# Kernel tuning notes

Hardware: AMD Instinct MI355X
Metric: run time of the kernel (lower is better)

Reference implementation:

```python
import jax, jax.numpy as jnp
import numpy as np

NUM_NODES = 500000
DIM = 128
BATCH = 131072
MOMENTUM = 0.9


def setup_inputs() -> dict:
    key = jax.random.key(0)
    ks = jax.random.split(key, 6)
    s = 1.0 / np.sqrt(DIM)
    return {
        "hidden": jax.random.normal(ks[0], (NUM_NODES, DIM), jnp.float32),
        "variance": jnp.ones((NUM_NODES, DIM), jnp.float32),
        "idx": jnp.arange(BATCH, dtype=jnp.int64 if jax.config.jax_enable_x64 else jnp.int32),
        "new_repr": jax.random.normal(ks[1], (BATCH, DIM), jnp.float32),
        "W_ih": jax.random.normal(ks[2], (3 * DIM, DIM), jnp.float32) * s,
        "W_hh": jax.random.normal(ks[3], (3 * DIM, DIM), jnp.float32) * s,
        "b_ih": jax.random.normal(ks[4], (3 * DIM,), jnp.float32) * s,
        "b_hh": jax.random.normal(ks[5], (3 * DIM,), jnp.float32) * s,
    }


def _gru_cell(x, h, W_ih, W_hh, b_ih, b_hh):
    # torch GRUCell gate layout: [reset | update | new], each of size DIM
    gi = x @ W_ih.T + b_ih          # [B, 3*DIM]
    gh = h @ W_hh.T + b_hh          # [B, 3*DIM]
    gi_r, gi_z, gi_n = jnp.split(gi, 3, axis=-1)
    gh_r, gh_z, gh_n = jnp.split(gh, 3, axis=-1)
    r = jax.nn.sigmoid(gi_r + gh_r)
    z = jax.nn.sigmoid(gi_z + gh_z)
    n = jnp.tanh(gi_n + r * gh_n)
    return (1.0 - z) * n + z * h


def reference(hidden, variance, idx, new_repr, W_ih, W_hh, b_ih, b_hh):
    h_prev = hidden[idx]                                   # gather [B, DIM]
    h_new = _gru_cell(new_repr, h_prev, W_ih, W_hh, b_ih, b_hh)
    delta = h_new - h_prev
    var_new = MOMENTUM * variance[idx] + (1.0 - MOMENTUM) * delta * delta
    hidden_out = hidden.at[idx].set(h_new)                 # scatter write
    variance_out = variance.at[idx].set(var_new)
    return jnp.stack([hidden_out, variance_out])           # [2, N, DIM]
```

## Files before the change

### kernel.cpp

```cpp
#include <hip/hip_runtime.h>
#include <hip/hip_bf16.h>
#include <cstdint>
#include <cstddef>

#define NUM_NODES 500000
#define DIM 128
#define BATCH 131072
#define NBLK (NUM_NODES / 32)

typedef __attribute__((ext_vector_type(8))) short short8;
typedef __attribute__((ext_vector_type(4))) short short4_t;
typedef __attribute__((ext_vector_type(4))) float f32x4;

static __device__ __forceinline__ short f2bf(float f) {
    unsigned u = __builtin_bit_cast(unsigned, f);
    u += 0x7fffu + ((u >> 16) & 1u);
    return (short)(u >> 16);
}
static __device__ __forceinline__ float bf2f(short s) {
    unsigned u = ((unsigned)(unsigned short)s) << 16;
    return __builtin_bit_cast(float, u);
}
static __device__ __forceinline__ f32x4 ntl(const float* p) {
    return __builtin_nontemporal_load((const f32x4*)p);
}
static __device__ __forceinline__ void nts(float* p, f32x4 v) {
    __builtin_nontemporal_store(v, (f32x4*)p);
}

__global__ void k_init(int* __restrict__ inv,
                       unsigned char* __restrict__ mask,
                       const float* __restrict__ Wih,
                       const float* __restrict__ Whh,
                       short* __restrict__ WbIH,
                       short* __restrict__ WbHH) {
    int i = blockIdx.x * blockDim.x + threadIdx.x;
    if (i < NUM_NODES) {
        if (inv)  inv[i] = -1;
        if (mask) mask[i] = 0;
    }
    if (i < 3 * DIM * DIM) {
        WbIH[i] = f2bf(Wih[i]);
        WbHH[i] = f2bf(Whh[i]);
    }
}

__global__ void k_scatter(int* __restrict__ inv, unsigned char* __restrict__ mask,
                          const int* __restrict__ idx) {
    int i = blockIdx.x * blockDim.x + threadIdx.x;
    if (i < BATCH) {
        int n = idx[i];
        if (inv)  inv[n] = i;
        if (mask) mask[n] = 1;
    }
}

__global__ void __launch_bounds__(512)
k_stream(const float* __restrict__ hidden,
         const float* __restrict__ variance,
         const int*   __restrict__ inv,
         const float* __restrict__ xg,
         const short* __restrict__ WbIH,
         const short* __restrict__ WbHH,
         const float* __restrict__ b_ih,
         const float* __restrict__ b_hh,
         float* __restrict__ out0,
         float* __restrict__ out1) {
    __shared__ __align__(16) char smem[26112];
    short (*Xb)[136] = (short(*)[136])smem;
    short (*Hb)[136] = (short(*)[136])(smem + 8704);
    short (*Vb)[136] = (short(*)[136])(smem + 17408);
    short (*Hn)[136] = (short(*)[136])smem;
    __shared__ int rinfo[32];
    __shared__ int hasUpd;

    const int t  = threadIdx.x;
    const int pb = (int)(((unsigned)blockIdx.x * 4099u) % 15625u);
    const int rb = pb * 32;

    if (t == 0) hasUpd = 0;
    if (t < 32) rinfo[t] = inv[rb + t];
    __syncthreads();
    if (t < 32 && rinfo[t] >= 0) hasUpd = 1;
    __syncthreads();

    if (!hasUpd) {
        #pragma unroll
        for (int jj = 0; jj < 2; ++jj) {
            int j = t + jj * 512;
            size_t off = (size_t)rb * DIM + j * 4;
            f32x4 h = ntl(hidden + off);
            f32x4 v = ntl(variance + off);
            nts(out0 + off, h);
            nts(out1 + off, v);
        }
        return;
    }

    #pragma unroll
    for (int jj = 0; jj < 2; ++jj) {
        int j = t + jj * 512;
        int row = j >> 5, c4 = j & 31;
        size_t off = (size_t)(rb + row) * DIM + c4 * 4;
        f32x4 hv = ntl(hidden + off);
        f32x4 vv = ntl(variance + off);
        int iv = rinfo[row];
        f32x4 xv = {0.f, 0.f, 0.f, 0.f};
        if (iv >= 0) {
            xv = ntl(xg + (size_t)iv * DIM + c4 * 4);
        } else {
            nts(out0 + off, hv);
            nts(out1 + off, vv);
        }
        short4_t xs, hs, vs;
        xs.x = f2bf(xv.x); xs.y = f2bf(xv.y); xs.z = f2bf(xv.z); xs.w = f2bf(xv.w);
        hs.x = f2bf(hv.x); hs.y = f2bf(hv.y); hs.z = f2bf(hv.z); hs.w = f2bf(hv.w);
        vs.x = f2bf(vv.x); vs.y = f2bf(vv.y); vs.z = f2bf(vv.z); vs.w = f2bf(vv.w);
        *(short4_t*)&Xb[row][c4 * 4] = xs;
        *(short4_t*)&Hb[row][c4 * 4] = hs;
        *(short4_t*)&Vb[row][c4 * 4] = vs;
    }
    __syncthreads();

    const int w  = t >> 6;
    const int l  = t & 63;
    const int c  = l & 15;
    const int gq = l >> 4;

    f32x4 acc[2][3][2] = {};

    #pragma unroll
    for (int ks = 0; ks < 4; ++ks) {
        const int k0 = ks * 32 + gq * 8;
        short8 a[2][2];
        a[0][0] = *(const short8*)&Xb[c][k0];
        a[1][0] = *(const short8*)&Xb[16 + c][k0];
        a[0][1] = *(const short8*)&Hb[c][k0];
        a[1][1] = *(const short8*)&Hb[16 + c][k0];
        #pragma unroll
        for (int th = 0; th < 3; ++th) {
            const int o = w * 16 + th * 128 + c;
            const short8 bi = *(const short8*)(WbIH + (size_t)o * DIM + k0);
            const short8 bh = *(const short8*)(WbHH + (size_t)o * DIM + k0);
            #pragma unroll
            for (int mt = 0; mt < 2; ++mt) {
                acc[mt][th][0] = __builtin_amdgcn_mfma_f32_16x16x32_bf16(a[mt][0], bi, acc[mt][th][0], 0, 0, 0);
                acc[mt][th][1] = __builtin_amdgcn_mfma_f32_16x16x32_bf16(a[mt][1], bh, acc[mt][th][1], 0, 0, 0);
            }
        }
    }
    __syncthreads();

    const int d = w * 16 + c;
    const float bs_r = b_ih[d]       + b_hh[d];
    const float bs_z = b_ih[d + 128] + b_hh[d + 128];
    const float bi_n = b_ih[d + 256];
    const float bh_n = b_hh[d + 256];

    #pragma unroll
    for (int mt = 0; mt < 2; ++mt) {
        #pragma unroll
        for (int r = 0; r < 4; ++r) {
            const int m = mt * 16 + gq * 4 + r;
            float s_r  = acc[mt][0][0][r] + acc[mt][0][1][r] + bs_r;
            float s_z  = acc[mt][1][0][r] + acc[mt][1][1][r] + bs_z;
            float gi_n = acc[mt][2][0][r] + bi_n;
            float gh_n = acc[mt][2][1][r] + bh_n;
            float rg = 1.f / (1.f + __expf(-s_r));
            float zg = 1.f / (1.f + __expf(-s_z));
            float aa = gi_n + rg * gh_n;
            float n  = 1.f - 2.f / (__expf(2.f * aa) + 1.f);
            float h  = bf2f(Hb[m][d]);
            Hn[m][d] = f2bf((1.f - zg) * n + zg * h);
        }
    }
    __syncthreads();

    #pragma unroll
    for (int jj = 0; jj < 2; ++jj) {
        int j = t + jj * 512;
        int row = j >> 5, c4 = j & 31;
        if (rinfo[row] < 0) continue;
        size_t off = (size_t)(rb + row) * DIM + c4 * 4;
        short4_t hns = *(short4_t*)&Hn[row][c4 * 4];
        short4_t hs  = *(short4_t*)&Hb[row][c4 * 4];
        short4_t vs  = *(short4_t*)&Vb[row][c4 * 4];
        f32x4 hn, var;
        hn.x = bf2f(hns.x); hn.y = bf2f(hns.y); hn.z = bf2f(hns.z); hn.w = bf2f(hns.w);
        float dx = hn.x - bf2f(hs.x), dy = hn.y - bf2f(hs.y);
        float dz = hn.z - bf2f(hs.z), dw = hn.w - bf2f(hs.w);
        var.x = 0.9f * bf2f(vs.x) + 0.1f * dx * dx;
        var.y = 0.9f * bf2f(vs.y) + 0.1f * dy * dy;
        var.z = 0.9f * bf2f(vs.z) + 0.1f * dz * dz;
        var.w = 0.9f * bf2f(vs.w) + 0.1f * dw * dw;
        nts(out0 + off, hn);
        nts(out1 + off, var);
    }
}

__global__ void __launch_bounds__(256)
k_copy(const float* __restrict__ hidden,
       const float* __restrict__ variance,
       const unsigned char* __restrict__ mask,
       float* __restrict__ out0,
       float* __restrict__ out1) {
    int gid = blockIdx.x * 256 + threadIdx.x;
    int row = gid >> 4;
    int c8  = gid & 15;
    if (mask && mask[row]) return;
    size_t off = (size_t)row * DIM + c8 * 8;
    f32x4 a0 = *(const f32x4*)(hidden + off);
    f32x4 a1 = *(const f32x4*)(hidden + off + 4);
    f32x4 b0 = *(const f32x4*)(variance + off);
    f32x4 b1 = *(const f32x4*)(variance + off + 4);
    *(f32x4*)(out0 + off)     = a0;
    *(f32x4*)(out0 + off + 4) = a1;
    *(f32x4*)(out1 + off)     = b0;
    *(f32x4*)(out1 + off + 4) = b1;
}

__global__ void __launch_bounds__(512)
k_gru(const float* __restrict__ hidden,
      const float* __restrict__ variance,
      const int*   __restrict__ idx,
      const float* __restrict__ xg,
      const short* __restrict__ WbIH,
      const short* __restrict__ WbHH,
      const float* __restrict__ b_ih,
      const float* __restrict__ b_hh,
      float* __restrict__ out0,
      float* __restrict__ out1) {
    __shared__ __align__(16) char smem[26112];
    short (*Xb)[136] = (short(*)[136])smem;
    short (*Hb)[136] = (short(*)[136])(smem + 8704);
    short (*Vb)[136] = (short(*)[136])(smem + 17408);
    short (*Hn)[136] = (short(*)[136])smem;

    const int t  = threadIdx.x;
    const int rb = blockIdx.x * 32;

    #pragma unroll
    for (int jj = 0; jj < 2; ++jj) {
        int j = t + jj * 512;
        int row = j >> 5, c4 = j & 31;
        int node = idx[rb + row];
        f32x4 xv = *(const f32x4*)(xg + (size_t)(rb + row) * DIM + c4 * 4);
        f32x4 hv = *(const f32x4*)(hidden + (size_t)node * DIM + c4 * 4);
        f32x4 vv = *(const f32x4*)(variance + (size_t)node * DIM + c4 * 4);
        short4_t xs, hs, vs;
        xs.x = f2bf(xv.x); xs.y = f2bf(xv.y); xs.z = f2bf(xv.z); xs.w = f2bf(xv.w);
        hs.x = f2bf(hv.x); hs.y = f2bf(hv.y); hs.z = f2bf(hv.z); hs.w = f2bf(hv.w);
        vs.x = f2bf(vv.x); vs.y = f2bf(vv.y); vs.z = f2bf(vv.z); vs.w = f2bf(vv.w);
        *(short4_t*)&Xb[row][c4 * 4] = xs;
        *(short4_t*)&Hb[row][c4 * 4] = hs;
        *(short4_t*)&Vb[row][c4 * 4] = vs;
    }
    __syncthreads();

    const int w  = t >> 6;
    const int l  = t & 63;
    const int c  = l & 15;
    const int gq = l >> 4;

    f32x4 acc[2][3][2] = {};
    #pragma unroll
    for (int ks = 0; ks < 4; ++ks) {
        const int k0 = ks * 32 + gq * 8;
        short8 a[2][2];
        a[0][0] = *(const short8*)&Xb[c][k0];
        a[1][0] = *(const short8*)&Xb[16 + c][k0];
        a[0][1] = *(const short8*)&Hb[c][k0];
        a[1][1] = *(const short8*)&Hb[16 + c][k0];
        #pragma unroll
        for (int th = 0; th < 3; ++th) {
            const int o = w * 16 + th * 128 + c;
            const short8 bi = *(const short8*)(WbIH + (size_t)o * DIM + k0);
            const short8 bh = *(const short8*)(WbHH + (size_t)o * DIM + k0);
            #pragma unroll
            for (int mt = 0; mt < 2; ++mt) {
                acc[mt][th][0] = __builtin_amdgcn_mfma_f32_16x16x32_bf16(a[mt][0], bi, acc[mt][th][0], 0, 0, 0);
                acc[mt][th][1] = __builtin_amdgcn_mfma_f32_16x16x32_bf16(a[mt][1], bh, acc[mt][th][1], 0, 0, 0);
            }
        }
    }
    __syncthreads();

    const int d = w * 16 + c;
    const float bs_r = b_ih[d]       + b_hh[d];
    const float bs_z = b_ih[d + 128] + b_hh[d + 128];
    const float bi_n = b_ih[d + 256];
    const float bh_n = b_hh[d + 256];
    #pragma unroll
    for (int mt = 0; mt < 2; ++mt) {
        #pragma unroll
        for (int r = 0; r < 4; ++r) {
            const int m = mt * 16 + gq * 4 + r;
            float s_r  = acc[mt][0][0][r] + acc[mt][0][1][r] + bs_r;
            float s_z  = acc[mt][1][0][r] + acc[mt][1][1][r] + bs_z;
            float gi_n = acc[mt][2][0][r] + bi_n;
            float gh_n = acc[mt][2][1][r] + bh_n;
            float rg = 1.f / (1.f + __expf(-s_r));
            float zg = 1.f / (1.f + __expf(-s_z));
            float aa = gi_n + rg * gh_n;
            float n  = 1.f - 2.f / (__expf(2.f * aa) + 1.f);
            float h  = bf2f(Hb[m][d]);
            Hn[m][d] = f2bf((1.f - zg) * n + zg * h);
        }
    }
    __syncthreads();

    #pragma unroll
    for (int jj = 0; jj < 2; ++jj) {
        int j = t + jj * 512;
        int row = j >> 5, c4 = j & 31;
        int node = idx[rb + row];
        size_t off = (size_t)node * DIM + c4 * 4;
        short4_t hns = *(short4_t*)&Hn[row][c4 * 4];
        short4_t hs  = *(short4_t*)&Hb[row][c4 * 4];
        short4_t vs  = *(short4_t*)&Vb[row][c4 * 4];
        f32x4 hn, var;
        hn.x = bf2f(hns.x); hn.y = bf2f(hns.y); hn.z = bf2f(hns.z); hn.w = bf2f(hns.w);
        float dx = hn.x - bf2f(hs.x), dy = hn.y - bf2f(hs.y);
        float dz = hn.z - bf2f(hs.z), dw = hn.w - bf2f(hs.w);
        var.x = 0.9f * bf2f(vs.x) + 0.1f * dx * dx;
        var.y = 0.9f * bf2f(vs.y) + 0.1f * dy * dy;
        var.z = 0.9f * bf2f(vs.z) + 0.1f * dz * dz;
        var.w = 0.9f * bf2f(vs.w) + 0.1f * dw * dw;
        *(f32x4*)(out0 + off) = hn;
        *(f32x4*)(out1 + off) = var;
    }
}

extern "C" void kernel_launch(void* const* d_in, const int* in_sizes, int n_in,
                              void* d_out, int out_size, void* d_ws, size_t ws_size,
                              hipStream_t stream) {
    const float* hidden   = (const float*)d_in[0];
    const float* variance = (const float*)d_in[1];
    const int*   idx      = (const int*)d_in[2];
    const float* x        = (const float*)d_in[3];
    const float* Wih      = (const float*)d_in[4];
    const float* Whh      = (const float*)d_in[5];
    const float* bih      = (const float*)d_in[6];
    const float* bhh      = (const float*)d_in[7];
    float* out0 = (float*)d_out;
    float* out1 = out0 + (size_t)NUM_NODES * DIM;

    const size_t invB  = (size_t)NUM_NODES * 4;
    const size_t maskB = (size_t)NUM_NODES;
    const size_t wB    = (size_t)3 * DIM * DIM * 2;

    const bool full = ws_size >= invB + 2 * wB;
    const bool mid  = !full && ws_size >= maskB + 16 + 2 * wB;

    if (full) {
        int*   inv  = (int*)d_ws;
        short* WbIH = (short*)((char*)d_ws + invB);
        short* WbHH = WbIH + 3 * DIM * DIM;
        k_init<<<(NUM_NODES + 255) / 256, 256, 0, stream>>>(
            inv, nullptr, Wih, Whh, WbIH, WbHH);
        k_scatter<<<BATCH / 256, 256, 0, stream>>>(inv, nullptr, idx);
        k_stream<<<NBLK, 512, 0, stream>>>(hidden, variance, inv, x,
                                           WbIH, WbHH, bih, bhh, out0, out1);
    } else if (mid) {
        unsigned char* mask = (unsigned char*)d_ws;
        short* WbIH = (short*)((char*)d_ws + ((maskB + 15) & ~size_t(15)));
        short* WbHH = WbIH + 3 * DIM * DIM;
        k_init<<<(NUM_NODES + 255) / 256, 256, 0, stream>>>(
            nullptr, mask, Wih, Whh, WbIH, WbHH);
        k_scatter<<<BATCH / 256, 256, 0, stream>>>(nullptr, mask, idx);
        k_copy<<<(NUM_NODES * 16) / 256, 256, 0, stream>>>(
            hidden, variance, mask, out0, out1);
        k_gru<<<BATCH / 32, 512, 0, stream>>>(hidden, variance, idx, x,
                                              WbIH, WbHH, bih, bhh, out0, out1);
    } else {
        short* WbIH = (short*)d_ws;
        short* WbHH = WbIH + 3 * DIM * DIM;
        k_init<<<(NUM_NODES + 255) / 256, 256, 0, stream>>>(
            nullptr, nullptr, Wih, Whh, WbIH, WbHH);
        k_copy<<<(NUM_NODES * 16) / 256, 256, 0, stream>>>(
            hidden, variance, nullptr, out0, out1);
        k_gru<<<BATCH / 32, 512, 0, stream>>>(hidden, variance, idx, x,
                                              WbIH, WbHH, bih, bhh, out0, out1);
    }
}
```

Baseline: 253.2 us.

## Fuse GRU epilogue writes into MFMA output layout, drop variance staging

The GRU gate epilogue now writes h_new and the updated variance directly from the MFMA accumulator layout, reading fp32 hidden/variance from global memory per element. This removes the Vb shared buffer, the Hn staging pass and two block barriers. Variance is now loaded only for non-updated rows in the staging loop. The hidden load becomes a regular cached load so the epilogue re-read can hit cache. The trade-off is that stores become scalar and strided per lane (one float per row/column) instead of coalesced 16-byte stores, which may reduce write efficiency.

```diff
diff --git a/kernel.cpp b/kernel.cpp
--- a/kernel.cpp
+++ b/kernel.cpp
@@ -66,11 +66,8 @@
          const float* __restrict__ b_hh,
          float* __restrict__ out0,
          float* __restrict__ out1) {
-    __shared__ __align__(16) char smem[26112];
-    short (*Xb)[136] = (short(*)[136])smem;
-    short (*Hb)[136] = (short(*)[136])(smem + 8704);
-    short (*Vb)[136] = (short(*)[136])(smem + 17408);
-    short (*Hn)[136] = (short(*)[136])smem;
+    __shared__ __align__(16) short Xb[32][136];
+    __shared__ __align__(16) short Hb[32][136];
     __shared__ int rinfo[32];
     __shared__ int hasUpd;
 
@@ -102,23 +99,21 @@
         int j = t + jj * 512;
         int row = j >> 5, c4 = j & 31;
         size_t off = (size_t)(rb + row) * DIM + c4 * 4;
-        f32x4 hv = ntl(hidden + off);
-        f32x4 vv = ntl(variance + off);
+        f32x4 hv = *(const f32x4*)(hidden + off);
         int iv = rinfo[row];
         f32x4 xv = {0.f, 0.f, 0.f, 0.f};
         if (iv >= 0) {
             xv = ntl(xg + (size_t)iv * DIM + c4 * 4);
         } else {
+            f32x4 vv = ntl(variance + off);
             nts(out0 + off, hv);
             nts(out1 + off, vv);
         }
-        short4_t xs, hs, vs;
+        short4_t xs, hs;
         xs.x = f2bf(xv.x); xs.y = f2bf(xv.y); xs.z = f2bf(xv.z); xs.w = f2bf(xv.w);
         hs.x = f2bf(hv.x); hs.y = f2bf(hv.y); hs.z = f2bf(hv.z); hs.w = f2bf(hv.w);
-        vs.x = f2bf(vv.x); vs.y = f2bf(vv.y); vs.z = f2bf(vv.z); vs.w = f2bf(vv.w);
         *(short4_t*)&Xb[row][c4 * 4] = xs;
         *(short4_t*)&Hb[row][c4 * 4] = hs;
-        *(short4_t*)&Vb[row][c4 * 4] = vs;
     }
     __syncthreads();
 
@@ -149,7 +144,6 @@
             }
         }
     }
-    __syncthreads();
 
     const int d = w * 16 + c;
     const float bs_r = b_ih[d]       + b_hh[d];
@@ -162,6 +156,8 @@
         #pragma unroll
         for (int r = 0; r < 4; ++r) {
             const int m = mt * 16 + gq * 4 + r;
+            if (rinfo[m] < 0) continue;
+            size_t off = (size_t)(rb + m) * DIM + d;
             float s_r  = acc[mt][0][0][r] + acc[mt][0][1][r] + bs_r;
             float s_z  = acc[mt][1][0][r] + acc[mt][1][1][r] + bs_z;
             float gi_n = acc[mt][2][0][r] + bi_n;
@@ -170,31 +166,13 @@
             float zg = 1.f / (1.f + __expf(-s_z));
             float aa = gi_n + rg * gh_n;
             float n  = 1.f - 2.f / (__expf(2.f * aa) + 1.f);
-            float h  = bf2f(Hb[m][d]);
-            Hn[m][d] = f2bf((1.f - zg) * n + zg * h);
-        }
-    }
-    __syncthreads();
-
-    #pragma unroll
-    for (int jj = 0; jj < 2; ++jj) {
-        int j = t + jj * 512;
-        int row = j >> 5, c4 = j & 31;
-        if (rinfo[row] < 0) continue;
-        size_t off = (size_t)(rb + row) * DIM + c4 * 4;
-        short4_t hns = *(short4_t*)&Hn[row][c4 * 4];
-        short4_t hs  = *(short4_t*)&Hb[row][c4 * 4];
-        short4_t vs  = *(short4_t*)&Vb[row][c4 * 4];
-        f32x4 hn, var;
-        hn.x = bf2f(hns.x); hn.y = bf2f(hns.y); hn.z = bf2f(hns.z); hn.w = bf2f(hns.w);
-        float dx = hn.x - bf2f(hs.x), dy = hn.y - bf2f(hs.y);
-        float dz = hn.z - bf2f(hs.z), dw = hn.w - bf2f(hs.w);
-        var.x = 0.9f * bf2f(vs.x) + 0.1f * dx * dx;
-        var.y = 0.9f * bf2f(vs.y) + 0.1f * dy * dy;
-        var.z = 0.9f * bf2f(vs.z) + 0.1f * dz * dz;
-        var.w = 0.9f * bf2f(vs.w) + 0.1f * dw * dw;
-        nts(out0 + off, hn);
-        nts(out1 + off, var);
+            float h  = hidden[off];
+            float v  = __builtin_nontemporal_load(variance + off);
+            float hn = (1.f - zg) * n + zg * h;
+            float dl = hn - h;
+            __builtin_nontemporal_store(hn, out0 + off);
+            __builtin_nontemporal_store(0.9f * v + 0.1f * dl * dl, out1 + off);
+        }
     }
 }
 
```

Result: slower. 280.8 us (+10.9%).

## Process 64 rows per block, defer variance load, restructure gate-wise MFMA loop

Applied to the files above, without the earlier changes.

Doubles the tile to 64 node rows per block, so each weight fragment loaded from global memory feeds four M-tiles instead of two, and blocks become fewer and larger. Variance is no longer staged in LDS as bf16; updated rows read it directly from global memory in the epilogue, which also uses full-precision variance. The MFMA loop now runs one gate at a time, computing reset and update sigmoids as each finishes, which keeps the live accumulator set small despite the larger tile. In exchange, the mixed pass-through/update path covers more rows, a tail block with bounds checks is added, and the block permutation changes.

```diff
diff --git a/kernel.cpp b/kernel.cpp
--- a/kernel.cpp
+++ b/kernel.cpp
@@ -6,7 +6,8 @@
 #define NUM_NODES 500000
 #define DIM 128
 #define BATCH 131072
-#define NBLK (NUM_NODES / 32)
+#define ROWS 64
+#define NBLK ((NUM_NODES + ROWS - 1) / ROWS)
 
 typedef __attribute__((ext_vector_type(8))) short short8;
 typedef __attribute__((ext_vector_type(4))) short short4_t;
@@ -66,28 +67,26 @@
          const float* __restrict__ b_hh,
          float* __restrict__ out0,
          float* __restrict__ out1) {
-    __shared__ __align__(16) char smem[26112];
-    short (*Xb)[136] = (short(*)[136])smem;
-    short (*Hb)[136] = (short(*)[136])(smem + 8704);
-    short (*Vb)[136] = (short(*)[136])(smem + 17408);
-    short (*Hn)[136] = (short(*)[136])smem;
-    __shared__ int rinfo[32];
+    __shared__ __align__(16) short Xb[ROWS][136];
+    __shared__ __align__(16) short Hb[ROWS][136];
+    short (*Hn)[136] = Xb;
+    __shared__ int rinfo[ROWS];
     __shared__ int hasUpd;
 
     const int t  = threadIdx.x;
-    const int pb = (int)(((unsigned)blockIdx.x * 4099u) % 15625u);
-    const int rb = pb * 32;
+    const int pb = (int)(((unsigned)blockIdx.x * 2003u) % (unsigned)NBLK);
+    const int rb = pb * ROWS;
+    const int nrows = min(ROWS, NUM_NODES - rb);
 
     if (t == 0) hasUpd = 0;
-    if (t < 32) rinfo[t] = inv[rb + t];
-    __syncthreads();
-    if (t < 32 && rinfo[t] >= 0) hasUpd = 1;
+    if (t < ROWS) rinfo[t] = (t < nrows) ? inv[rb + t] : -1;
+    __syncthreads();
+    if (t < ROWS && rinfo[t] >= 0) hasUpd = 1;
     __syncthreads();
 
     if (!hasUpd) {
-        #pragma unroll
-        for (int jj = 0; jj < 2; ++jj) {
-            int j = t + jj * 512;
+        const int nchunks = nrows * 32;
+        for (int j = t; j < nchunks; j += 512) {
             size_t off = (size_t)rb * DIM + j * 4;
             f32x4 h = ntl(hidden + off);
             f32x4 v = ntl(variance + off);
@@ -98,27 +97,27 @@
     }
 
     #pragma unroll
-    for (int jj = 0; jj < 2; ++jj) {
+    for (int jj = 0; jj < 4; ++jj) {
         int j = t + jj * 512;
         int row = j >> 5, c4 = j & 31;
-        size_t off = (size_t)(rb + row) * DIM + c4 * 4;
-        f32x4 hv = ntl(hidden + off);
-        f32x4 vv = ntl(variance + off);
-        int iv = rinfo[row];
-        f32x4 xv = {0.f, 0.f, 0.f, 0.f};
-        if (iv >= 0) {
-            xv = ntl(xg + (size_t)iv * DIM + c4 * 4);
-        } else {
-            nts(out0 + off, hv);
-            nts(out1 + off, vv);
-        }
-        short4_t xs, hs, vs;
-        xs.x = f2bf(xv.x); xs.y = f2bf(xv.y); xs.z = f2bf(xv.z); xs.w = f2bf(xv.w);
-        hs.x = f2bf(hv.x); hs.y = f2bf(hv.y); hs.z = f2bf(hv.z); hs.w = f2bf(hv.w);
-        vs.x = f2bf(vv.x); vs.y = f2bf(vv.y); vs.z = f2bf(vv.z); vs.w = f2bf(vv.w);
+        short4_t xs = {0, 0, 0, 0}, hs = {0, 0, 0, 0};
+        if (row < nrows) {
+            size_t off = (size_t)(rb + row) * DIM + c4 * 4;
+            f32x4 hv = ntl(hidden + off);
+            int iv = rinfo[row];
+            f32x4 xv = {0.f, 0.f, 0.f, 0.f};
+            if (iv >= 0) {
+                xv = ntl(xg + (size_t)iv * DIM + c4 * 4);
+            } else {
+                f32x4 vv = ntl(variance + off);
+                nts(out0 + off, hv);
+                nts(out1 + off, vv);
+            }
+            xs.x = f2bf(xv.x); xs.y = f2bf(xv.y); xs.z = f2bf(xv.z); xs.w = f2bf(xv.w);
+            hs.x = f2bf(hv.x); hs.y = f2bf(hv.y); hs.z = f2bf(hv.z); hs.w = f2bf(hv.w);
+        }
         *(short4_t*)&Xb[row][c4 * 4] = xs;
         *(short4_t*)&Hb[row][c4 * 4] = hs;
-        *(short4_t*)&Vb[row][c4 * 4] = vs;
     }
     __syncthreads();
 
@@ -126,30 +125,6 @@
     const int l  = t & 63;
     const int c  = l & 15;
     const int gq = l >> 4;
-
-    f32x4 acc[2][3][2] = {};
-
-    #pragma unroll
-    for (int ks = 0; ks < 4; ++ks) {
-        const int k0 = ks * 32 + gq * 8;
-        short8 a[2][2];
-        a[0][0] = *(const short8*)&Xb[c][k0];
-        a[1][0] = *(const short8*)&Xb[16 + c][k0];
-        a[0][1] = *(const short8*)&Hb[c][k0];
-        a[1][1] = *(const short8*)&Hb[16 + c][k0];
-        #pragma unroll
-        for (int th = 0; th < 3; ++th) {
-            const int o = w * 16 + th * 128 + c;
-            const short8 bi = *(const short8*)(WbIH + (size_t)o * DIM + k0);
-            const short8 bh = *(const short8*)(WbHH + (size_t)o * DIM + k0);
-            #pragma unroll
-            for (int mt = 0; mt < 2; ++mt) {
-                acc[mt][th][0] = __builtin_amdgcn_mfma_f32_16x16x32_bf16(a[mt][0], bi, acc[mt][th][0], 0, 0, 0);
-                acc[mt][th][1] = __builtin_amdgcn_mfma_f32_16x16x32_bf16(a[mt][1], bh, acc[mt][th][1], 0, 0, 0);
-            }
-        }
-    }
-    __syncthreads();
 
     const int d = w * 16 + c;
     const float bs_r = b_ih[d]       + b_hh[d];
@@ -157,42 +132,71 @@
     const float bi_n = b_ih[d + 256];
     const float bh_n = b_hh[d + 256];
 
-    #pragma unroll
-    for (int mt = 0; mt < 2; ++mt) {
+    float rg[4][4], zg[4][4];
+
+    #pragma unroll
+    for (int th = 0; th < 3; ++th) {
+        f32x4 acc[4][2] = {};
+        const int o = w * 16 + th * 128 + c;
         #pragma unroll
-        for (int r = 0; r < 4; ++r) {
-            const int m = mt * 16 + gq * 4 + r;
-            float s_r  = acc[mt][0][0][r] + acc[mt][0][1][r] + bs_r;
-            float s_z  = acc[mt][1][0][r] + acc[mt][1][1][r] + bs_z;
-            float gi_n = acc[mt][2][0][r] + bi_n;
-            float gh_n = acc[mt][2][1][r] + bh_n;
-            float rg = 1.f / (1.f + __expf(-s_r));
-            float zg = 1.f / (1.f + __expf(-s_z));
-            float aa = gi_n + rg * gh_n;
-            float n  = 1.f - 2.f / (__expf(2.f * aa) + 1.f);
-            float h  = bf2f(Hb[m][d]);
-            Hn[m][d] = f2bf((1.f - zg) * n + zg * h);
-        }
-    }
-    __syncthreads();
-
-    #pragma unroll
-    for (int jj = 0; jj < 2; ++jj) {
+        for (int ks = 0; ks < 4; ++ks) {
+            const int k0 = ks * 32 + gq * 8;
+            const short8 bi = *(const short8*)(WbIH + (size_t)o * DIM + k0);
+            const short8 bh = *(const short8*)(WbHH + (size_t)o * DIM + k0);
+            #pragma unroll
+            for (int mt = 0; mt < 4; ++mt) {
+                const short8 aX = *(const short8*)&Xb[mt * 16 + c][k0];
+                const short8 aH = *(const short8*)&Hb[mt * 16 + c][k0];
+                acc[mt][0] = __builtin_amdgcn_mfma_f32_16x16x32_bf16(aX, bi, acc[mt][0], 0, 0, 0);
+                acc[mt][1] = __builtin_amdgcn_mfma_f32_16x16x32_bf16(aH, bh, acc[mt][1], 0, 0, 0);
+            }
+        }
+        if (th == 0) {
+            #pragma unroll
+            for (int mt = 0; mt < 4; ++mt)
+                #pragma unroll
+                for (int r = 0; r < 4; ++r)
+                    rg[mt][r] = 1.f / (1.f + __expf(-(acc[mt][0][r] + acc[mt][1][r] + bs_r)));
+        } else if (th == 1) {
+            #pragma unroll
+            for (int mt = 0; mt < 4; ++mt)
+                #pragma unroll
+                for (int r = 0; r < 4; ++r)
+                    zg[mt][r] = 1.f / (1.f + __expf(-(acc[mt][0][r] + acc[mt][1][r] + bs_z)));
+        } else {
+            __syncthreads();
+            #pragma unroll
+            for (int mt = 0; mt < 4; ++mt) {
+                #pragma unroll
+                for (int r = 0; r < 4; ++r) {
+                    const int m = mt * 16 + gq * 4 + r;
+                    float aa = (acc[mt][0][r] + bi_n) + rg[mt][r] * (acc[mt][1][r] + bh_n);
+                    float n  = 1.f - 2.f / (__expf(2.f * aa) + 1.f);
+                    float h  = bf2f(Hb[m][d]);
+                    Hn[m][d] = f2bf((1.f - zg[mt][r]) * n + zg[mt][r] * h);
+                }
+            }
+        }
+    }
+    __syncthreads();
+
+    #pragma unroll
+    for (int jj = 0; jj < 4; ++jj) {
         int j = t + jj * 512;
         int row = j >> 5, c4 = j & 31;
-        if (rinfo[row] < 0) continue;
+        if (row >= nrows || rinfo[row] < 0) continue;
         size_t off = (size_t)(rb + row) * DIM + c4 * 4;
         short4_t hns = *(short4_t*)&Hn[row][c4 * 4];
         short4_t hs  = *(short4_t*)&Hb[row][c4 * 4];
-        short4_t vs  = *(short4_t*)&Vb[row][c4 * 4];
+        f32x4 vv = ntl(variance + off);
         f32x4 hn, var;
         hn.x = bf2f(hns.x); hn.y = bf2f(hns.y); hn.z = bf2f(hns.z); hn.w = bf2f(hns.w);
         float dx = hn.x - bf2f(hs.x), dy = hn.y - bf2f(hs.y);
         float dz = hn.z - bf2f(hs.z), dw = hn.w - bf2f(hs.w);
-        var.x = 0.9f * bf2f(vs.x) + 0.1f * dx * dx;
-        var.y = 0.9f * bf2f(vs.y) + 0.1f * dy * dy;
-        var.z = 0.9f * bf2f(vs.z) + 0.1f * dz * dz;
-        var.w = 0.9f * bf2f(vs.w) + 0.1f * dw * dw;
+        var.x = 0.9f * vv.x + 0.1f * dx * dx;
+        var.y = 0.9f * vv.y + 0.1f * dy * dy;
+        var.z = 0.9f * vv.z + 0.1f * dz * dz;
+        var.w = 0.9f * vv.w + 0.1f * dw * dw;
         nts(out0 + off, hn);
         nts(out1 + off, var);
     }
```

Measured after the change: 287.2 us. 13.4% more time.
